# Kernel optimization log

Measured on AMD Instinct MI355X. Metric: run time of the kernel, lower is better.

The kernel has to match this reference:

```python
import jax, jax.numpy as jnp
import numpy as np

N = 262144   # collocation points (512x512 grid equivalent)
H = 64       # MLP hidden width
PI = np.float32(np.pi)


def setup_inputs() -> dict:
    key = jax.random.key(0)
    ks = jax.random.split(key, 6)
    def glorot(k, shp):
        scale = np.float32(np.sqrt(2.0 / (shp[0] + shp[1])))
        return jax.random.normal(k, shp, jnp.float32) * scale
    return {
        "points": jax.random.uniform(ks[0], (N, 2), jnp.float32),  # (x, t) in [0,1]^2
        "W1": glorot(ks[1], (2, H)), "b1": jnp.zeros((H,), jnp.float32),
        "W2": glorot(ks[2], (H, H)), "b2": jnp.zeros((H,), jnp.float32),
        "W3": glorot(ks[3], (H, H)), "b3": jnp.zeros((H,), jnp.float32),
        "Wo": glorot(ks[4], (H, 1)), "bo": jnp.zeros((1,), jnp.float32),
    }


def _mlp(pt, W1, b1, W2, b2, W3, b3, Wo, bo):
    # pt: [2] -> scalar u(x, t)
    h = jnp.tanh(pt @ W1 + b1)
    h = jnp.tanh(h @ W2 + b2)
    h = jnp.tanh(h @ W3 + b3)
    return (h @ Wo + bo)[0]


def reference(points, W1, b1, W2, b2, W3, b3, Wo, bo):
    params = (W1, b1, W2, b2, W3, b3, Wo, bo)
    dt = points.dtype
    keep_t = jnp.array([0.0, 1.0], dt)   # points * [0,1]
    set_x1 = jnp.array([1.0, 0.0], dt)   # + [1,0] -> (1, t)

    def psi_fn(pt):
        x, t = pt[0], pt[1]
        pt1t = pt * keep_t + set_x1                    # boundary point (1, t)
        u = _mlp(pt, *params)                          # u(x, t)
        u_1t = _mlp(pt1t, *params)                     # u(1, t)
        u1t_x = jax.grad(lambda p: _mlp(p, *params))(pt1t)[0]  # du/dx at (1, t)
        return (2.0 * x * jnp.sin(PI * t)
                + (t * t - t) * (x * x - x) * (u - u_1t - u1t_x))

    def loss_point(pt):
        x, t = pt[0], pt[1]
        psi, g1 = jax.value_and_grad(psi_fn)(pt)       # g1 = (psi_x, psi_t)
        # TF's tape.gradient sums over components of dpsi_dxdt, so:
        # h = grad(psi_x + psi_t) = (psi_xx + psi_tx, psi_xt + psi_tt)
        h = jax.grad(lambda p: jnp.sum(jax.grad(psi_fn)(p)))(pt)
        s = jnp.sin(PI * t)
        res = (h[0] + h[1] + psi * g1[0]
               - s * (2.0 - PI * PI * x * x + 2.0 * x ** 3 * s))
        return jnp.abs(res)

    return jnp.mean(jax.vmap(loss_point)(points))
```

## Files before the change

kernel.cpp:

```cpp
#include <hip/hip_runtime.h>
#include <math.h>

typedef _Float16 half_t;
typedef half_t half8 __attribute__((ext_vector_type(8)));
typedef __fp16 fp16x2 __attribute__((ext_vector_type(2)));
typedef float f32x4 __attribute__((ext_vector_type(4)));
typedef float f32x2 __attribute__((ext_vector_type(2)));

#define PI_F 3.14159265358979323846f

__device__ __forceinline__ f32x2 splat2(float s) { return f32x2{s, s}; }
__device__ __forceinline__ f32x2 fma2(f32x2 a, f32x2 b, f32x2 c) {
    return __builtin_elementwise_fma(a, b, c);
}

__device__ __forceinline__ f32x2 ftanh2(f32x2 z) {
    const f32x2 m = z * splat2(2.8853900817779268f);
    f32x2 t;
    t[0] = exp2f(m[0]);
    t[1] = exp2f(m[1]);
    f32x2 r;
    r[0] = __builtin_amdgcn_rcpf(t[0] + 1.f);
    r[1] = __builtin_amdgcn_rcpf(t[1] + 1.f);
    return (t - splat2(1.f)) * r;
}


__global__ __launch_bounds__(256) void pinn_main(
    const float* __restrict__ pts,
    const float* __restrict__ W1, const float* __restrict__ b1,
    const float* __restrict__ b2, const float* __restrict__ b3,
    const half_t* __restrict__ wsH,
    float* __restrict__ partial)
{
    __shared__ __align__(16) half_t J[192 * 64];
    __shared__ float ubuf[12][16];

    const int tid = threadIdx.x;
    const int l   = tid & 63;
    const int w   = tid >> 6;
    const int q   = l >> 4;
    const int i   = l & 15;
    const int ja  = w * 16 + i;
    const int jb  = w * 16 + q * 4;

    const int rb0 = i * 64 + ((q ^ (i & 7)) << 3);
    const int rb1 = i * 64 + (((4 + q) ^ (i & 7)) << 3);
    const int wbase = i * 64 + ((((w * 2 + (q >> 1)) ^ (i & 7))) << 3) + (q & 1) * 4;

    const half8 w2a = *(const half8*)(wsH + ja * 64 + q * 8);
    const half8 w2b = *(const half8*)(wsH + ja * 64 + 32 + q * 8);
    const half8 w3a = *(const half8*)(wsH + 4096 + ja * 64 + q * 8);
    const half8 w3b = *(const half8*)(wsH + 4096 + ja * 64 + 32 + q * 8);

    const float4 w04 = *(const float4*)(W1 + jb);
    const float4 w14 = *(const float4*)(W1 + 64 + jb);
    const float4 b14 = *(const float4*)(b1 + jb);
    const float4 b24 = *(const float4*)(b2 + jb);
    const float4 b34 = *(const float4*)(b3 + jb);

    half8 wo0 = {0, 0, 0, 0, 0, 0, 0, 0};
    half8 wo1 = {0, 0, 0, 0, 0, 0, 0, 0};
    if (i == 0) {
        wo0 = *(const half8*)(wsH + 8192 + q * 8);
        wo1 = *(const half8*)(wsH + 8192 + 32 + q * 8);
    }

    auto stc = [&](int c, f32x2 v01, f32x2 v23) {
        uint2 d;
        d.x = __builtin_bit_cast(unsigned int,
                                 __builtin_amdgcn_cvt_pkrtz(v01[0], v01[1]));
        d.y = __builtin_bit_cast(unsigned int,
                                 __builtin_amdgcn_cvt_pkrtz(v23[0], v23[1]));
        *(uint2*)(&J[wbase + c * 1024]) = d;
    };

    const f32x2 w0a = {w04.x, w04.y}, w0b = {w04.z, w04.w};
    const f32x2 w1a = {w14.x, w14.y}, w1b = {w14.z, w14.w};
    const f32x2 bba = {b14.x, b14.y}, bbb = {b14.z, b14.w};

    float bsum = 0.f;

    #pragma unroll 1
    for (int pass = 0; pass < 2; ++pass) {
        const int pbase = blockIdx.x * 32 + pass * 16;

        const float2 xy = *(const float2*)(pts + 2 * (pbase + i));
        const float X = xy.x, T = xy.y;

        {
            const f32x2 zva = fma2(splat2(X), w0a, fma2(splat2(T), w1a, bba));
            const f32x2 zvb = fma2(splat2(X), w0b, fma2(splat2(T), w1b, bbb));
            const f32x2 aa = ftanh2(zva), ab = ftanh2(zvb);
            const f32x2 d1a = splat2(1.f) - aa * aa, d1b = splat2(1.f) - ab * ab;
            const f32x2 d2a = splat2(-2.f) * aa * d1a, d2b = splat2(-2.f) * ab * d1b;
            stc(0, aa, ab);
            stc(1, d1a * w0a, d1b * w0b);
            stc(2, d1a * w1a, d1b * w1b);
            stc(3, d2a * w0a * w0a, d2b * w0b * w0b);
            stc(4, d2a * w0a * w1a, d2b * w0b * w1b);
            stc(5, d2a * w1a * w1a, d2b * w1b * w1b);
        }
        {
            const f32x2 zva = fma2(splat2(T), w1a, bba + w0a);
            const f32x2 zvb = fma2(splat2(T), w1b, bbb + w0b);
            const f32x2 aa = ftanh2(zva), ab = ftanh2(zvb);
            const f32x2 e1a = splat2(1.f) - aa * aa, e1b = splat2(1.f) - ab * ab;
            const f32x2 e2a = splat2(-2.f) * aa * e1a, e2b = splat2(-2.f) * ab * e1b;
            const f32x2 e3a = splat2(-2.f) * (e1a * e1a + aa * e2a);
            const f32x2 e3b = splat2(-2.f) * (e1b * e1b + ab * e2b);
            stc(6, aa, ab);
            stc(7, e1a * w0a, e1b * w0b);
            stc(8, e1a * w1a, e1b * w1b);
            stc(9, e2a * w0a * w1a, e2b * w0b * w1b);
            stc(10, e2a * w1a * w1a, e2b * w1b * w1b);
            stc(11, e3a * w0a * w1a * w1a, e3b * w0b * w1b * w1b);
        }

        auto layer_step = [&](const half8 A0, const half8 A1, const float4 b4) {
            __syncthreads();
            const f32x4 zb = {b4.x, b4.y, b4.z, b4.w};
            const f32x4 z0 = {0.f, 0.f, 0.f, 0.f};
            f32x4 acc[12];
            #pragma unroll
            for (int c = 0; c < 12; ++c) {
                const half8 f0 = *(const half8*)(&J[rb0 + c * 1024]);
                const half8 f1 = *(const half8*)(&J[rb1 + c * 1024]);
                f32x4 z = (c == 0 || c == 6) ? zb : z0;
                z = __builtin_amdgcn_mfma_f32_16x16x32_f16(A0, f0, z, 0, 0, 0);
                z = __builtin_amdgcn_mfma_f32_16x16x32_f16(A1, f1, z, 0, 0, 0);
                acc[c] = z;
            }
            __syncthreads();

            {
                const f32x2 zva = {acc[0][0], acc[0][1]}, zvb = {acc[0][2], acc[0][3]};
                const f32x2 aa = ftanh2(zva), ab = ftanh2(zvb);
                const f32x2 d1a = splat2(1.f) - aa * aa, d1b = splat2(1.f) - ab * ab;
                const f32x2 d2a = splat2(-2.f) * aa * d1a, d2b = splat2(-2.f) * ab * d1b;
                const f32x2 zxa = {acc[1][0], acc[1][1]}, zxb = {acc[1][2], acc[1][3]};
                const f32x2 zta = {acc[2][0], acc[2][1]}, ztb = {acc[2][2], acc[2][3]};
                const f32x2 zxxa = {acc[3][0], acc[3][1]}, zxxb = {acc[3][2], acc[3][3]};
                const f32x2 zxta = {acc[4][0], acc[4][1]}, zxtb = {acc[4][2], acc[4][3]};
                const f32x2 ztta = {acc[5][0], acc[5][1]}, zttb = {acc[5][2], acc[5][3]};
                stc(0, aa, ab);
                stc(1, d1a * zxa, d1b * zxb);
                stc(2, d1a * zta, d1b * ztb);
                stc(3, fma2(d2a * zxa, zxa, d1a * zxxa), fma2(d2b * zxb, zxb, d1b * zxxb));
                stc(4, fma2(d2a * zxa, zta, d1a * zxta), fma2(d2b * zxb, ztb, d1b * zxtb));
                stc(5, fma2(d2a * zta, zta, d1a * ztta), fma2(d2b * ztb, ztb, d1b * zttb));
            }
            {
                const f32x2 zva = {acc[6][0], acc[6][1]}, zvb = {acc[6][2], acc[6][3]};
                const f32x2 aa = ftanh2(zva), ab = ftanh2(zvb);
                const f32x2 e1a = splat2(1.f) - aa * aa, e1b = splat2(1.f) - ab * ab;
                const f32x2 e2a = splat2(-2.f) * aa * e1a, e2b = splat2(-2.f) * ab * e1b;
                const f32x2 e3a = splat2(-2.f) * (e1a * e1a + aa * e2a);
                const f32x2 e3b = splat2(-2.f) * (e1b * e1b + ab * e2b);
                const f32x2 zxa  = {acc[7][0], acc[7][1]},  zxb  = {acc[7][2], acc[7][3]};
                const f32x2 zta  = {acc[8][0], acc[8][1]},  ztb  = {acc[8][2], acc[8][3]};
                const f32x2 zxta = {acc[9][0], acc[9][1]},  zxtb = {acc[9][2], acc[9][3]};
                const f32x2 ztta = {acc[10][0], acc[10][1]}, zttb = {acc[10][2], acc[10][3]};
                const f32x2 zxtta = {acc[11][0], acc[11][1]}, zxttb = {acc[11][2], acc[11][3]};
                stc(6, aa, ab);
                stc(7, e1a * zxa, e1b * zxb);
                stc(8, e1a * zta, e1b * ztb);
                stc(9, fma2(e2a * zxa, zta, e1a * zxta), fma2(e2b * zxb, ztb, e1b * zxtb));
                stc(10, fma2(e2a * zta, zta, e1a * ztta), fma2(e2b * ztb, ztb, e1b * zttb));
                stc(11,
                    fma2(e3a * zxa, zta * zta,
                         fma2(e2a, fma2(splat2(2.f) * zxta, zta, zxa * ztta), e1a * zxtta)),
                    fma2(e3b * zxb, ztb * ztb,
                         fma2(e2b, fma2(splat2(2.f) * zxtb, ztb, zxb * zttb), e1b * zxttb)));
            }
        };
        layer_step(w2a, w2b, b24);
        layer_step(w3a, w3b, b34);
        __syncthreads();

        {
            const int rbg0 = rb0 + w * 3 * 1024;
            const int rbg1 = rb1 + w * 3 * 1024;
            #pragma unroll
            for (int k3 = 0; k3 < 3; ++k3) {
                const half8 f0 = *(const half8*)(&J[rbg0 + k3 * 1024]);
                const half8 f1 = *(const half8*)(&J[rbg1 + k3 * 1024]);
                f32x4 z = {0.f, 0.f, 0.f, 0.f};
                z = __builtin_amdgcn_mfma_f32_16x16x32_f16(wo0, f0, z, 0, 0, 0);
                z = __builtin_amdgcn_mfma_f32_16x16x32_f16(wo1, f1, z, 0, 0, 0);
                if (q == 0) ubuf[w * 3 + k3][i] = z[0];
            }
        }
        __syncthreads();

        if (tid < 16) {
            const float x = X, t = T;
            float U[12];
            #pragma unroll
            for (int c = 0; c < 12; ++c) U[c] = ubuf[c][tid];

            const float D   = U[0] - U[6] - U[7];
            const float Dx  = U[1];
            const float Dt  = U[2] - U[8] - U[9];
            const float Dxx = U[3];
            const float Dxt = U[4];
            const float Dtt = U[5] - U[10] - U[11];

            const float s  = __builtin_amdgcn_sinf(0.5f * t);
            const float cc = __builtin_amdgcn_cosf(0.5f * t);
            const float A  = t * t - t,  Ap = 2.f * t - 1.f;
            const float B  = x * x - x,  Bp = 2.f * x - 1.f;

            const float psi    = 2.f * x * s + A * B * D;
            const float psi_x  = 2.f * s + A * (Bp * D + B * Dx);
            const float psi_xx = A * (2.f * D + 2.f * Bp * Dx + B * Dxx);
            const float psi_xt = 2.f * PI_F * cc + Ap * (Bp * D + B * Dx)
                               + A * (Bp * Dt + B * Dxt);
            const float psi_tt = -2.f * PI_F * PI_F * x * s + 2.f * B * D
                               + 2.f * Ap * B * Dt + A * B * Dtt;

            const float forcing = s * (2.f - PI_F * PI_F * x * x
                                       + 2.f * x * x * x * s);
            float s4 = fabsf(psi_xx + 2.f * psi_xt + psi_tt + psi * psi_x - forcing);
            s4 += __shfl_xor(s4, 1, 64);
            s4 += __shfl_xor(s4, 2, 64);
            s4 += __shfl_xor(s4, 4, 64);
            s4 += __shfl_xor(s4, 8, 64);
            if (tid == 0) bsum += s4;
        }
    }

    if (tid == 0) partial[blockIdx.x] = bsum;
}

__global__ __launch_bounds__(256) void pinn_prep(
    const float* __restrict__ W2, const float* __restrict__ W3,
    const float* __restrict__ Wo, half_t* __restrict__ wsH)
{
    const int tid = threadIdx.x;
    for (int idx = tid; idx < 4096; idx += 256) {
        const int n = idx >> 6, k = idx & 63;
        wsH[idx]        = (half_t)W2[k * 64 + n];
        wsH[4096 + idx] = (half_t)W3[k * 64 + n];
    }
    if (tid < 64) wsH[8192 + tid] = (half_t)Wo[tid];
}

__global__ __launch_bounds__(256) void pinn_reduce(
    const float* __restrict__ partial, float* __restrict__ out,
    int nblocks, float invN)
{
    __shared__ float sd[256];
    float s = 0.f;
    for (int i = threadIdx.x; i < nblocks; i += 256) s += partial[i];
    sd[threadIdx.x] = s;
    __syncthreads();
    #pragma unroll
    for (int off = 128; off > 0; off >>= 1) {
        if (threadIdx.x < off) sd[threadIdx.x] += sd[threadIdx.x + off];
        __syncthreads();
    }
    if (threadIdx.x == 0) out[0] = sd[0] * invN;
}

extern "C" void kernel_launch(void* const* d_in, const int* in_sizes, int n_in,
                              void* d_out, int out_size, void* d_ws, size_t ws_size,
                              hipStream_t stream)
{
    const float* pts = (const float*)d_in[0];
    const float* W1  = (const float*)d_in[1];
    const float* b1  = (const float*)d_in[2];
    const float* W2  = (const float*)d_in[3];
    const float* b2  = (const float*)d_in[4];
    const float* W3  = (const float*)d_in[5];
    const float* b3  = (const float*)d_in[6];
    const float* Wo  = (const float*)d_in[7];

    const int nPts    = in_sizes[0] / 2;
    const int nBlocks = nPts / 32;

    half_t* wsH     = (half_t*)d_ws;
    float*  partial = (float*)((char*)d_ws + 32768);

    pinn_prep<<<1, 256, 0, stream>>>(W2, W3, Wo, wsH);
    pinn_main<<<nBlocks, 256, 0, stream>>>(pts, W1, b1, b2, b3, wsH, partial);
    pinn_reduce<<<1, 256, 0, stream>>>(partial, (float*)d_out, nBlocks,
                                       1.f / (float)nPts);
}
```

Baseline: 131.9 us.

## Double-buffer LDS Jacobian, merge boundary channels before output layer, simplify tanh

Splits the shared Jacobian buffer into two ping-pong halves so each layer reads from one and writes to the other. This removes one __syncthreads per layer step. In the last hidden layer, the boundary channel pairs that are later subtracted together are summed before storing. The output projection then covers 9 channels instead of 12 and runs on only three warps. tanh is rewritten as 1 - 2/(e^{2z}+1), which saves a subtraction and a multiply. The cost is double the LDS footprint, which may lower occupancy, plus extra fp16 rounding from summing channels before conversion.

```diff
diff --git a/kernel.cpp b/kernel.cpp
--- a/kernel.cpp
+++ b/kernel.cpp
@@ -8,6 +8,7 @@
 typedef float f32x2 __attribute__((ext_vector_type(2)));
 
 #define PI_F 3.14159265358979323846f
+#define JSZ (192 * 64)
 
 __device__ __forceinline__ f32x2 splat2(float s) { return f32x2{s, s}; }
 __device__ __forceinline__ f32x2 fma2(f32x2 a, f32x2 b, f32x2 c) {
@@ -19,12 +20,12 @@
     f32x2 t;
     t[0] = exp2f(m[0]);
     t[1] = exp2f(m[1]);
+    const f32x2 s = t + splat2(1.f);
     f32x2 r;
-    r[0] = __builtin_amdgcn_rcpf(t[0] + 1.f);
-    r[1] = __builtin_amdgcn_rcpf(t[1] + 1.f);
-    return (t - splat2(1.f)) * r;
-}
-
+    r[0] = __builtin_amdgcn_rcpf(s[0]);
+    r[1] = __builtin_amdgcn_rcpf(s[1]);
+    return fma2(splat2(-2.f), r, splat2(1.f));
+}
 
 __global__ __launch_bounds__(256) void pinn_main(
     const float* __restrict__ pts,
@@ -33,8 +34,8 @@
     const half_t* __restrict__ wsH,
     float* __restrict__ partial)
 {
-    __shared__ __align__(16) half_t J[192 * 64];
-    __shared__ float ubuf[12][16];
+    __shared__ __align__(16) half_t J[2][JSZ];
+    __shared__ float ubuf[9][16];
 
     const int tid = threadIdx.x;
     const int l   = tid & 63;
@@ -66,13 +67,13 @@
         wo1 = *(const half8*)(wsH + 8192 + 32 + q * 8);
     }
 
-    auto stc = [&](int c, f32x2 v01, f32x2 v23) {
+    auto stc = [&](half_t* dst, int c, f32x2 v01, f32x2 v23) {
         uint2 d;
         d.x = __builtin_bit_cast(unsigned int,
                                  __builtin_amdgcn_cvt_pkrtz(v01[0], v01[1]));
         d.y = __builtin_bit_cast(unsigned int,
                                  __builtin_amdgcn_cvt_pkrtz(v23[0], v23[1]));
-        *(uint2*)(&J[wbase + c * 1024]) = d;
+        *(uint2*)(&dst[wbase + c * 1024]) = d;
     };
 
     const f32x2 w0a = {w04.x, w04.y}, w0b = {w04.z, w04.w};
@@ -87,6 +88,9 @@
 
         const float2 xy = *(const float2*)(pts + 2 * (pbase + i));
         const float X = xy.x, T = xy.y;
+
+        half_t* JA = &J[0][0];
+        half_t* JB = &J[1][0];
 
         {
             const f32x2 zva = fma2(splat2(X), w0a, fma2(splat2(T), w1a, bba));
@@ -94,12 +98,12 @@
             const f32x2 aa = ftanh2(zva), ab = ftanh2(zvb);
             const f32x2 d1a = splat2(1.f) - aa * aa, d1b = splat2(1.f) - ab * ab;
             const f32x2 d2a = splat2(-2.f) * aa * d1a, d2b = splat2(-2.f) * ab * d1b;
-            stc(0, aa, ab);
-            stc(1, d1a * w0a, d1b * w0b);
-            stc(2, d1a * w1a, d1b * w1b);
-            stc(3, d2a * w0a * w0a, d2b * w0b * w0b);
-            stc(4, d2a * w0a * w1a, d2b * w0b * w1b);
-            stc(5, d2a * w1a * w1a, d2b * w1b * w1b);
+            stc(JA, 0, aa, ab);
+            stc(JA, 1, d1a * w0a, d1b * w0b);
+            stc(JA, 2, d1a * w1a, d1b * w1b);
+            stc(JA, 3, d2a * w0a * w0a, d2b * w0b * w0b);
+            stc(JA, 4, d2a * w0a * w1a, d2b * w0b * w1b);
+            stc(JA, 5, d2a * w1a * w1a, d2b * w1b * w1b);
         }
         {
             const f32x2 zva = fma2(splat2(T), w1a, bba + w0a);
@@ -109,29 +113,30 @@
             const f32x2 e2a = splat2(-2.f) * aa * e1a, e2b = splat2(-2.f) * ab * e1b;
             const f32x2 e3a = splat2(-2.f) * (e1a * e1a + aa * e2a);
             const f32x2 e3b = splat2(-2.f) * (e1b * e1b + ab * e2b);
-            stc(6, aa, ab);
-            stc(7, e1a * w0a, e1b * w0b);
-            stc(8, e1a * w1a, e1b * w1b);
-            stc(9, e2a * w0a * w1a, e2b * w0b * w1b);
-            stc(10, e2a * w1a * w1a, e2b * w1b * w1b);
-            stc(11, e3a * w0a * w1a * w1a, e3b * w0b * w1b * w1b);
+            stc(JA, 6, aa, ab);
+            stc(JA, 7, e1a * w0a, e1b * w0b);
+            stc(JA, 8, e1a * w1a, e1b * w1b);
+            stc(JA, 9, e2a * w0a * w1a, e2b * w0b * w1b);
+            stc(JA, 10, e2a * w1a * w1a, e2b * w1b * w1b);
+            stc(JA, 11, e3a * w0a * w1a * w1a, e3b * w0b * w1b * w1b);
         }
-
-        auto layer_step = [&](const half8 A0, const half8 A1, const float4 b4) {
-            __syncthreads();
+        __syncthreads();
+
+        auto layer_step = [&](const half_t* src, half_t* dst,
+                              const half8 A0, const half8 A1,
+                              const float4 b4, bool combine) {
             const f32x4 zb = {b4.x, b4.y, b4.z, b4.w};
             const f32x4 z0 = {0.f, 0.f, 0.f, 0.f};
             f32x4 acc[12];
             #pragma unroll
             for (int c = 0; c < 12; ++c) {
-                const half8 f0 = *(const half8*)(&J[rb0 + c * 1024]);
-                const half8 f1 = *(const half8*)(&J[rb1 + c * 1024]);
+                const half8 f0 = *(const half8*)(&src[rb0 + c * 1024]);
+                const half8 f1 = *(const half8*)(&src[rb1 + c * 1024]);
                 f32x4 z = (c == 0 || c == 6) ? zb : z0;
                 z = __builtin_amdgcn_mfma_f32_16x16x32_f16(A0, f0, z, 0, 0, 0);
                 z = __builtin_amdgcn_mfma_f32_16x16x32_f16(A1, f1, z, 0, 0, 0);
                 acc[c] = z;
             }
-            __syncthreads();
 
             {
                 const f32x2 zva = {acc[0][0], acc[0][1]}, zvb = {acc[0][2], acc[0][3]};
@@ -143,12 +148,15 @@
                 const f32x2 zxxa = {acc[3][0], acc[3][1]}, zxxb = {acc[3][2], acc[3][3]};
                 const f32x2 zxta = {acc[4][0], acc[4][1]}, zxtb = {acc[4][2], acc[4][3]};
                 const f32x2 ztta = {acc[5][0], acc[5][1]}, zttb = {acc[5][2], acc[5][3]};
-                stc(0, aa, ab);
-                stc(1, d1a * zxa, d1b * zxb);
-                stc(2, d1a * zta, d1b * ztb);
-                stc(3, fma2(d2a * zxa, zxa, d1a * zxxa), fma2(d2b * zxb, zxb, d1b * zxxb));
-                stc(4, fma2(d2a * zxa, zta, d1a * zxta), fma2(d2b * zxb, ztb, d1b * zxtb));
-                stc(5, fma2(d2a * zta, zta, d1a * ztta), fma2(d2b * ztb, ztb, d1b * zttb));
+                stc(dst, 0, aa, ab);
+                stc(dst, 1, d1a * zxa, d1b * zxb);
+                stc(dst, 2, d1a * zta, d1b * ztb);
+                stc(dst, 3, fma2(d2a * zxa, zxa, d1a * zxxa),
+                            fma2(d2b * zxb, zxb, d1b * zxxb));
+                stc(dst, 4, fma2(d2a * zxa, zta, d1a * zxta),
+                            fma2(d2b * zxb, ztb, d1b * zxtb));
+                stc(dst, 5, fma2(d2a * zta, zta, d1a * ztta),
+                            fma2(d2b * ztb, ztb, d1b * zttb));
             }
             {
                 const f32x2 zva = {acc[6][0], acc[6][1]}, zvb = {acc[6][2], acc[6][3]};
@@ -162,49 +170,64 @@
                 const f32x2 zxta = {acc[9][0], acc[9][1]},  zxtb = {acc[9][2], acc[9][3]};
                 const f32x2 ztta = {acc[10][0], acc[10][1]}, zttb = {acc[10][2], acc[10][3]};
                 const f32x2 zxtta = {acc[11][0], acc[11][1]}, zxttb = {acc[11][2], acc[11][3]};
-                stc(6, aa, ab);
-                stc(7, e1a * zxa, e1b * zxb);
-                stc(8, e1a * zta, e1b * ztb);
-                stc(9, fma2(e2a * zxa, zta, e1a * zxta), fma2(e2b * zxb, ztb, e1b * zxtb));
-                stc(10, fma2(e2a * zta, zta, e1a * ztta), fma2(e2b * ztb, ztb, e1b * zttb));
-                stc(11,
+                const f32x2 o6a = aa,            o6b = ab;
+                const f32x2 o7a = e1a * zxa,     o7b = e1b * zxb;
+                const f32x2 o8a = e1a * zta,     o8b = e1b * ztb;
+                const f32x2 o9a  = fma2(e2a * zxa, zta, e1a * zxta);
+                const f32x2 o9b  = fma2(e2b * zxb, ztb, e1b * zxtb);
+                const f32x2 o10a = fma2(e2a * zta, zta, e1a * ztta);
+                const f32x2 o10b = fma2(e2b * ztb, ztb, e1b * zttb);
+                const f32x2 o11a =
                     fma2(e3a * zxa, zta * zta,
-                         fma2(e2a, fma2(splat2(2.f) * zxta, zta, zxa * ztta), e1a * zxtta)),
+                         fma2(e2a, fma2(splat2(2.f) * zxta, zta, zxa * ztta), e1a * zxtta));
+                const f32x2 o11b =
                     fma2(e3b * zxb, ztb * ztb,
-                         fma2(e2b, fma2(splat2(2.f) * zxtb, ztb, zxb * zttb), e1b * zxttb)));
+                         fma2(e2b, fma2(splat2(2.f) * zxtb, ztb, zxb * zttb), e1b * zxttb));
+                if (combine) {
+                    stc(dst, 6, o6a + o7a,  o6b + o7b);
+                    stc(dst, 7, o8a + o9a,  o8b + o9b);
+                    stc(dst, 8, o10a + o11a, o10b + o11b);
+                } else {
+                    stc(dst, 6, o6a, o6b);
+                    stc(dst, 7, o7a, o7b);
+                    stc(dst, 8, o8a, o8b);
+                    stc(dst, 9, o9a, o9b);
+                    stc(dst, 10, o10a, o10b);
+                    stc(dst, 11, o11a, o11b);
+                }
             }
         };
-        layer_step(w2a, w2b, b24);
-        layer_step(w3a, w3b, b34);
-        __syncthreads();
-
-        {
-            const int rbg0 = rb0 + w * 3 * 1024;
-            const int rbg1 = rb1 + w * 3 * 1024;
+        layer_step(JA, JB, w2a, w2b, b24, false);
+        __syncthreads();
+        layer_step(JB, JA, w3a, w3b, b34, true);
+        __syncthreads();
+
+        if (w < 3) {
             #pragma unroll
             for (int k3 = 0; k3 < 3; ++k3) {
-                const half8 f0 = *(const half8*)(&J[rbg0 + k3 * 1024]);
-                const half8 f1 = *(const half8*)(&J[rbg1 + k3 * 1024]);
+                const int c = w * 3 + k3;
+                const half8 f0 = *(const half8*)(&JA[rb0 + c * 1024]);
+                const half8 f1 = *(const half8*)(&JA[rb1 + c * 1024]);
                 f32x4 z = {0.f, 0.f, 0.f, 0.f};
                 z = __builtin_amdgcn_mfma_f32_16x16x32_f16(wo0, f0, z, 0, 0, 0);
                 z = __builtin_amdgcn_mfma_f32_16x16x32_f16(wo1, f1, z, 0, 0, 0);
-                if (q == 0) ubuf[w * 3 + k3][i] = z[0];
+                if (q == 0) ubuf[c][i] = z[0];
             }
         }
         __syncthreads();
 
         if (tid < 16) {
             const float x = X, t = T;
-            float U[12];
+            float U[9];
             #pragma unroll
-            for (int c = 0; c < 12; ++c) U[c] = ubuf[c][tid];
-
-            const float D   = U[0] - U[6] - U[7];
+            for (int c = 0; c < 9; ++c) U[c] = ubuf[c][tid];
+
+            const float D   = U[0] - U[6];
             const float Dx  = U[1];
-            const float Dt  = U[2] - U[8] - U[9];
+            const float Dt  = U[2] - U[7];
             const float Dxx = U[3];
             const float Dxt = U[4];
-            const float Dtt = U[5] - U[10] - U[11];
+            const float Dtt = U[5] - U[8];
 
             const float s  = __builtin_amdgcn_sinf(0.5f * t);
             const float cc = __builtin_amdgcn_cosf(0.5f * t);
```

After: 151.6 us. 14.9% more time.
